# Kernel tuning notes

Measured on AMD Instinct MI355X. Metric: run time of the kernel, lower is better.

The kernel has to match this reference:

```python
import jax, jax.numpy as jnp
import numpy as np

M = 5  # init kwarg of InterestCandidateAttention


def setup_inputs() -> dict:
    key = jax.random.key(0)
    k1, k2, k3 = jax.random.split(key, 3)
    bs, K, d = 4096, 50, 256
    interest = jax.random.normal(k1, (bs, K, d), dtype=jnp.float32)
    candidate = jax.random.normal(k2, (bs, d), dtype=jnp.float32)
    counts = jax.random.randint(k3, (bs,), 1, 20, dtype=jnp.int64)
    return {
        "interest_representations": interest,
        "candidate_news_representation": candidate,
        "unique_category_counts": counts,
    }


def reference(interest_representations, candidate_news_representation, unique_category_counts):
    bs, K, d = interest_representations.shape
    # per-row dot-product scores: [bs, K]
    attn = jnp.einsum("bkd,bd->bk", interest_representations, candidate_news_representation)
    # dynamic K per sample: ceil(log2(M * count)) clamped to [1, K]
    counts = jnp.maximum(unique_category_counts, 1).astype(jnp.float32)
    dyn_K = jnp.clip(jnp.ceil(jnp.log2(M * counts)).astype(jnp.int32), 1, K)  # [bs]
    # rank-based top-k mask (vectorized replacement of per-sample topk loop)
    order = jnp.argsort(-attn, axis=-1)          # indices sorted by descending score
    ranks = jnp.argsort(order, axis=-1)          # rank of each element (0 = largest)
    mask = (ranks < dyn_K[:, None]).astype(attn.dtype)  # [bs, K]
    masked = attn * mask
    # masked weighted sum over interests -> [bs, d]
    user = jnp.einsum("bk,bkd->bd", masked, interest_representations)
    return user
```

## Files before the change

### kernel.cpp

```cpp
#include <hip/hip_runtime.h>

#define NK 50
#define D  256
#define NW 8
#define RPW 7

typedef float f4 __attribute__((ext_vector_type(4)));

__global__ __launch_bounds__(512, 8) void ica_kernel(
    const float* __restrict__ interest,
    const float* __restrict__ cand,
    const int*   __restrict__ counts,
    float*       __restrict__ out,
    int bs)
{
    const int b    = blockIdx.x;
    const int tid  = threadIdx.x;
    const int lane = tid & 63;
    const int wave = tid >> 6;

    __shared__ float s_attn[NK];
    __shared__ float s_w[NK];
    __shared__ float s_part[NW][D];

    const float* irow = interest + (size_t)b * NK * D;

    const f4 c4 = __builtin_nontemporal_load(
        reinterpret_cast<const f4*>(cand + (size_t)b * D + lane * 4));

    f4 frag[RPW];
    #pragma unroll
    for (int i = 0; i < RPW; ++i) {
        const int k = wave + i * NW;
        if (k < NK)
            frag[i] = __builtin_nontemporal_load(
                reinterpret_cast<const f4*>(irow + (size_t)k * D + lane * 4));
    }

    #pragma unroll
    for (int i = 0; i < RPW; ++i) {
        const int k = wave + i * NW;
        if (k < NK) {
            const f4 a4 = frag[i];
            float p = a4.x * c4.x + a4.y * c4.y + a4.z * c4.z + a4.w * c4.w;
            #pragma unroll
            for (int off = 32; off >= 1; off >>= 1)
                p += __shfl_xor(p, off, 64);
            if (lane == 0) s_attn[k] = p;
        }
    }
    __syncthreads();

    if (wave == 0) {
        int cnt = counts[b];
        if (cnt < 1) cnt = 1;
        int dynK = (int)ceilf(log2f(5.0f * (float)cnt));
        if (dynK < 1)  dynK = 1;
        if (dynK > NK) dynK = NK;

        if (lane < NK) {
            const float my = s_attn[lane];
            int rank = 0;
            #pragma unroll 1
            for (int j = 0; j < NK; ++j) {
                const float vj = s_attn[j];
                rank += (vj > my) || (vj == my && j < lane);
            }
            s_w[lane] = (rank < dynK) ? my : 0.0f;
        }
    }
    __syncthreads();

    f4 acc = {0.f, 0.f, 0.f, 0.f};
    #pragma unroll
    for (int i = 0; i < RPW; ++i) {
        const int k = wave + i * NW;
        if (k < NK) {
            const float w = s_w[k];
            acc.x += w * frag[i].x;
            acc.y += w * frag[i].y;
            acc.z += w * frag[i].z;
            acc.w += w * frag[i].w;
        }
    }
    *reinterpret_cast<f4*>(&s_part[wave][lane * 4]) = acc;
    __syncthreads();

    if (tid < D) {
        float r = 0.f;
        #pragma unroll
        for (int w = 0; w < NW; ++w)
            r += s_part[w][tid];
        out[(size_t)b * D + tid] = r;
    }
}

extern "C" void kernel_launch(void* const* d_in, const int* in_sizes, int n_in,
                              void* d_out, int out_size, void* d_ws, size_t ws_size,
                              hipStream_t stream) {
    const float* interest = (const float*)d_in[0];
    const float* cand     = (const float*)d_in[1];
    const int*   counts   = (const int*)d_in[2];
    float*       out      = (float*)d_out;

    const int bs = in_sizes[2];
    ica_kernel<<<bs, 512, 0, stream>>>(interest, cand, counts, out, bs);
}
```

Measured before the change: 38.83 us.

## Use persistent blocks with async global-to-LDS prefetch of next sample rows

Converts the one-block-per-sample launch into a persistent grid of at most 1024 blocks. Each block loops over samples with a grid-sized stride. While the current sample is processed, the first 24 interest rows of the next sample are prefetched into LDS with global_load_lds, and the remaining rows are loaded directly into registers. The aim is to hide memory latency and cut block launch overhead. In exchange it adds 24 KB of LDS per block, which may lower occupancy, and uses hand-written barriers with inline waitcnt that need careful ordering.

```diff
diff --git a/kernel.cpp b/kernel.cpp
--- a/kernel.cpp
+++ b/kernel.cpp
@@ -4,8 +4,85 @@
 #define D  256
 #define NW 8
 #define RPW 7
+#define PFR 24
+#define GRIDSZ 1024
 
 typedef float f4 __attribute__((ext_vector_type(4)));
+typedef const __attribute__((address_space(1))) void* as1cv;
+typedef __attribute__((address_space(3))) void*       as3v;
+
+__device__ __forceinline__ void glds16(const float* g, float* s) {
+    __builtin_amdgcn_global_load_lds((as1cv)g, (as3v)s, 16, 0, 0);
+}
+
+#define BAR_LGKM() asm volatile("s_waitcnt lgkmcnt(0)\n\ts_barrier" ::: "memory")
+#define BAR_ALL()  asm volatile("s_waitcnt vmcnt(0) lgkmcnt(0)\n\ts_barrier" ::: "memory")
+
+#define NTLOAD(p) __builtin_nontemporal_load(reinterpret_cast<const f4*>(p))
+
+#define DOTS()                                                          \
+    _Pragma("unroll")                                                   \
+    for (int i_ = 0; i_ < RPW; ++i_) {                                  \
+        const int k_ = wave + i_ * NW;                                  \
+        if (k_ < NK) {                                                  \
+            const f4 a_ = frag[i_];                                     \
+            float p_ = a_.x*c4.x + a_.y*c4.y + a_.z*c4.z + a_.w*c4.w;   \
+            _Pragma("unroll")                                           \
+            for (int o_ = 32; o_ >= 1; o_ >>= 1)                        \
+                p_ += __shfl_xor(p_, o_, 64);                           \
+            if (lane == 0) s_attn[k_] = p_;                             \
+        }                                                               \
+    }
+
+#define PREFETCH(SN)                                                    \
+    {                                                                   \
+        const float* ip_ = interest + (size_t)(SN) * (NK * D);          \
+        _Pragma("unroll")                                               \
+        for (int i_ = 0; i_ < 3; ++i_) {                                \
+            const int r_ = wave + i_ * NW;                              \
+            glds16(ip_ + (size_t)r_ * D + lane * 4, &s_buf[r_ * D]);    \
+        }                                                               \
+    }
+
+#define TAIL(S, CNT)                                                    \
+    {                                                                   \
+        if (wave == 0) {                                                \
+            int c_ = (CNT) < 1 ? 1 : (CNT);                             \
+            int dk_ = (int)ceilf(log2f(5.0f * (float)c_));              \
+            dk_ = dk_ < 1 ? 1 : (dk_ > NK ? NK : dk_);                  \
+            if (lane < NK) {                                            \
+                const float my_ = s_attn[lane];                         \
+                int rk_ = 0;                                            \
+                _Pragma("unroll 1")                                     \
+                for (int j_ = 0; j_ < NK; ++j_) {                       \
+                    const float vj_ = s_attn[j_];                       \
+                    rk_ += (vj_ > my_) || (vj_ == my_ && j_ < lane);    \
+                }                                                       \
+                s_w[lane] = (rk_ < dk_) ? my_ : 0.0f;                   \
+            }                                                           \
+        }                                                               \
+        BAR_LGKM();                                                     \
+        {                                                               \
+            f4 acc_ = {0.f, 0.f, 0.f, 0.f};                             \
+            _Pragma("unroll")                                           \
+            for (int i_ = 0; i_ < RPW; ++i_) {                          \
+                const int k_ = wave + i_ * NW;                          \
+                if (k_ < NK) {                                          \
+                    const float w_ = s_w[k_];                           \
+                    acc_.x += w_ * frag[i_].x;  acc_.y += w_ * frag[i_].y; \
+                    acc_.z += w_ * frag[i_].z;  acc_.w += w_ * frag[i_].w; \
+                }                                                       \
+            }                                                           \
+            *reinterpret_cast<f4*>(&s_part[wave][lane * 4]) = acc_;     \
+        }                                                               \
+        BAR_LGKM();                                                     \
+        if (tid < D) {                                                  \
+            float r_ = 0.f;                                             \
+            _Pragma("unroll")                                           \
+            for (int w_ = 0; w_ < NW; ++w_) r_ += s_part[w_][tid];      \
+            out[(size_t)(S) * D + tid] = r_;                            \
+        }                                                               \
+    }
 
 __global__ __launch_bounds__(512, 8) void ica_kernel(
     const float* __restrict__ interest,
@@ -14,84 +91,58 @@
     float*       __restrict__ out,
     int bs)
 {
-    const int b    = blockIdx.x;
     const int tid  = threadIdx.x;
     const int lane = tid & 63;
     const int wave = tid >> 6;
+    const int stride = gridDim.x;
 
     __shared__ float s_attn[NK];
     __shared__ float s_w[NK];
     __shared__ float s_part[NW][D];
+    __shared__ float s_buf[PFR * D];
 
-    const float* irow = interest + (size_t)b * NK * D;
+    int s = blockIdx.x;
+    f4  frag[RPW];
+    f4  c4;
+    int cnt;
 
-    const f4 c4 = __builtin_nontemporal_load(
-        reinterpret_cast<const f4*>(cand + (size_t)b * D + lane * 4));
+    {
+        const float* irow = interest + (size_t)s * (NK * D);
+        #pragma unroll
+        for (int i = 0; i < RPW; ++i) {
+            const int k = wave + i * NW;
+            if (k < NK) frag[i] = NTLOAD(irow + (size_t)k * D + lane * 4);
+        }
+        c4  = *reinterpret_cast<const f4*>(cand + (size_t)s * D + lane * 4);
+        cnt = counts[s];
+    }
+    int sn = s + stride;
+    if (sn < bs) PREFETCH(sn)
+    DOTS()
+    BAR_LGKM();
+    TAIL(s, cnt)
 
-    f4 frag[RPW];
-    #pragma unroll
-    for (int i = 0; i < RPW; ++i) {
-        const int k = wave + i * NW;
-        if (k < NK)
-            frag[i] = __builtin_nontemporal_load(
-                reinterpret_cast<const f4*>(irow + (size_t)k * D + lane * 4));
-    }
-
-    #pragma unroll
-    for (int i = 0; i < RPW; ++i) {
-        const int k = wave + i * NW;
-        if (k < NK) {
-            const f4 a4 = frag[i];
-            float p = a4.x * c4.x + a4.y * c4.y + a4.z * c4.z + a4.w * c4.w;
-            #pragma unroll
-            for (int off = 32; off >= 1; off >>= 1)
-                p += __shfl_xor(p, off, 64);
-            if (lane == 0) s_attn[k] = p;
+    #pragma unroll 1
+    while (sn < bs) {
+        BAR_ALL();
+        s = sn; sn = s + stride;
+        const float* irow = interest + (size_t)s * (NK * D);
+        #pragma unroll
+        for (int i = 3; i < RPW; ++i) {
+            const int k = wave + i * NW;
+            if (k < NK) frag[i] = NTLOAD(irow + (size_t)k * D + lane * 4);
         }
-    }
-    __syncthreads();
-
-    if (wave == 0) {
-        int cnt = counts[b];
-        if (cnt < 1) cnt = 1;
-        int dynK = (int)ceilf(log2f(5.0f * (float)cnt));
-        if (dynK < 1)  dynK = 1;
-        if (dynK > NK) dynK = NK;
-
-        if (lane < NK) {
-            const float my = s_attn[lane];
-            int rank = 0;
-            #pragma unroll 1
-            for (int j = 0; j < NK; ++j) {
-                const float vj = s_attn[j];
-                rank += (vj > my) || (vj == my && j < lane);
-            }
-            s_w[lane] = (rank < dynK) ? my : 0.0f;
+        c4  = *reinterpret_cast<const f4*>(cand + (size_t)s * D + lane * 4);
+        cnt = counts[s];
+        #pragma unroll
+        for (int i = 0; i < 3; ++i) {
+            const int r = wave + i * NW;
+            frag[i] = *reinterpret_cast<const f4*>(&s_buf[r * D + lane * 4]);
         }
-    }
-    __syncthreads();
-
-    f4 acc = {0.f, 0.f, 0.f, 0.f};
-    #pragma unroll
-    for (int i = 0; i < RPW; ++i) {
-        const int k = wave + i * NW;
-        if (k < NK) {
-            const float w = s_w[k];
-            acc.x += w * frag[i].x;
-            acc.y += w * frag[i].y;
-            acc.z += w * frag[i].z;
-            acc.w += w * frag[i].w;
-        }
-    }
-    *reinterpret_cast<f4*>(&s_part[wave][lane * 4]) = acc;
-    __syncthreads();
-
-    if (tid < D) {
-        float r = 0.f;
-        #pragma unroll
-        for (int w = 0; w < NW; ++w)
-            r += s_part[w][tid];
-        out[(size_t)b * D + tid] = r;
+        DOTS()
+        BAR_LGKM();
+        if (sn < bs) PREFETCH(sn)
+        TAIL(s, cnt)
     }
 }
 
@@ -103,6 +154,7 @@
     const int*   counts   = (const int*)d_in[2];
     float*       out      = (float*)d_out;
 
-    const int bs = in_sizes[2];
-    ica_kernel<<<bs, 512, 0, stream>>>(interest, cand, counts, out, bs);
+    const int bs   = in_sizes[2];
+    const int grid = (bs < GRIDSZ) ? bs : GRIDSZ;
+    ica_kernel<<<grid, 512, 0, stream>>>(interest, cand, counts, out, bs);
 }
```

After: 49.00 us. +26.2%, slower.
